# Kernel optimization log

Measured on AMD Instinct MI355X. Metric: run time of the kernel, lower is better.

## Reference

```python
import jax, jax.numpy as jnp
import numpy as np

K = 8192   # num_embeddings
D = 256    # embedding_dim


def setup_inputs() -> dict:
    key = jax.random.key(0)
    k1, k2 = jax.random.split(key)
    inputs = jax.random.normal(k1, (8, 4096, D), dtype=jnp.float32)
    # torch init: uniform_(-1/num_embeddings, 1/num_embeddings)
    embeddings_weight = jax.random.uniform(
        k2, (K, D), dtype=jnp.float32, minval=-1.0 / K, maxval=1.0 / K
    )
    return {"inputs": inputs, "embeddings_weight": embeddings_weight}


def reference(inputs, embeddings_weight):
    in_shape = inputs.shape
    flat = inputs.reshape(-1, D)                      # [N, D]
    distances = (
        jnp.sum(flat * flat, axis=1, keepdims=True)   # [N, 1]
        + jnp.sum(embeddings_weight * embeddings_weight, axis=1)  # [K]
        - 2.0 * jnp.matmul(flat, embeddings_weight.T)             # [N, K]
    )
    encoding_indices = jnp.argmin(distances, axis=1)  # [N] int
    # one-hot @ W is mathematically a row gather of W
    quantized = jnp.take(embeddings_weight, encoding_indices, axis=0).reshape(in_shape)
    return quantized, encoding_indices
```

## Files before the change

### kernel.cpp

```cpp
#include <hip/hip_runtime.h>
#include <cfloat>


#define DDIM 256

typedef int   i32x8  __attribute__((ext_vector_type(8)));
typedef float f32x16 __attribute__((ext_vector_type(16)));

__device__ __forceinline__ float np_sumsq_lane(const float* __restrict__ a) {
    float r = __fmul_rn(a[0], a[0]);
#pragma unroll
    for (int t = 1; t < 16; ++t)
        r = __fadd_rn(r, __fmul_rn(a[8 * t], a[8 * t]));
    return r;
}

__global__ __launch_bounds__(256) void vq_prep(
    const float* __restrict__ x, const float* __restrict__ w,
    float* __restrict__ x2, float* __restrict__ wn,
    unsigned char* __restrict__ xb8, unsigned char* __restrict__ wb8,
    int nxblocks) {
    __shared__ float rows[32 * 260];
    const int tid = threadIdx.x;
    const bool isX = (int)blockIdx.x < nxblocks;
    const int r0 = (isX ? blockIdx.x : (blockIdx.x - nxblocks)) * 32;
    const float* src = isX ? x : w;

    for (int idx = tid; idx < 32 * 64; idx += 256) {
        int r = idx >> 6, c4 = idx & 63;
        *(float4*)&rows[r * 260 + c4 * 4] =
            *(const float4*)(src + (size_t)(r0 + r) * DDIM + c4 * 4);
    }
    __syncthreads();
    {
        const int row = (tid >> 6) * 8 + ((tid & 63) >> 3), j = tid & 7;
        const float* a = &rows[row * 260];
        float half[2];
#pragma unroll
        for (int h = 0; h < 2; ++h) {
            float r = np_sumsq_lane(a + h * 128 + j);
            float p = __fadd_rn(r, __shfl_xor(r, 1, 64));
            p = __fadd_rn(p, __shfl_xor(p, 2, 64));
            p = __fadd_rn(p, __shfl_xor(p, 4, 64));
            half[h] = p;
        }
        float s = __fadd_rn(half[0], half[1]);
        if (j == 0) { if (isX) x2[r0 + row] = s; else wn[r0 + row] = s; }
    }
    {
        const float scale = isX ? 1.0f : -8192.0f;
        unsigned char* dst = isX ? xb8 : wb8;
        for (int idx = tid; idx < 32 * 16; idx += 256) {
            int r = idx >> 4, s = idx & 15;
            const float* p = &rows[r * 260 + s * 16];
            unsigned q[4];
#pragma unroll
            for (int m = 0; m < 4; ++m) {
                unsigned v = (unsigned)__builtin_amdgcn_cvt_pk_fp8_f32(
                    p[m * 4 + 0] * scale, p[m * 4 + 1] * scale, 0, false);
                v = (unsigned)__builtin_amdgcn_cvt_pk_fp8_f32(
                    p[m * 4 + 2] * scale, p[m * 4 + 3] * scale, (int)v, true);
                q[m] = v;
            }
            *(uint4*)(dst + (size_t)(r0 + r) * DDIM + s * 16) =
                make_uint4(q[0], q[1], q[2], q[3]);
        }
    }
}

__global__ __launch_bounds__(512, 1) void vq_score(
    const unsigned char* __restrict__ xb8, const unsigned char* __restrict__ wb8,
    unsigned* __restrict__ cand) {
    __shared__ __align__(16) unsigned char Ws[2][32768];
    const int tid = threadIdx.x;
    const int wave = tid >> 6, lane = tid & 63;
    const int h = lane >> 5, c32 = lane & 31;
    const int wr = wave >> 2, wc = wave & 3;
    const int rowBase = blockIdx.x * 128;

    i32x8 af[2][4];
#pragma unroll
    for (int rt = 0; rt < 2; ++rt) {
        const unsigned char* xr =
            xb8 + (size_t)(rowBase + wr * 64 + rt * 32 + c32) * DDIM;
#pragma unroll
        for (int ks = 0; ks < 4; ++ks) {
            union { uint4 q[2]; i32x8 v; } u;
            u.q[0] = *(const uint4*)(xr + ks * 64 + h * 32);
            u.q[1] = *(const uint4*)(xr + ks * 64 + h * 32 + 16);
            af[rt][ks] = u.v;
        }
    }

    unsigned sOfs[4]; unsigned ldsOfs[4];
#pragma unroll
    for (int i = 0; i < 4; ++i) {
        int col = (wave * 4 + i) * 4 + (lane >> 4);
        int gsrc = (lane & 15) ^ (col & 15);
        sOfs[i] = (unsigned)(col * 256 + gsrc * 16);
        ldsOfs[i] = (unsigned)((wave * 4 + i) * 1024);
    }

    unsigned s0[2][16], s1[2][16];
#pragma unroll
    for (int a = 0; a < 2; ++a)
#pragma unroll
        for (int r = 0; r < 16; ++r) { s0[a][r] = 0xFFFFFFFFu; s1[a][r] = 0xFFFFFFFFu; }

    const int bcol = wc * 32 + c32, cs = bcol & 15;
    int bofs[4][2];
#pragma unroll
    for (int ks = 0; ks < 4; ++ks) {
        int gb = ks * 4 + h * 2;
        bofs[ks][0] = bcol * 256 + ((gb) ^ cs) * 16;
        bofs[ks][1] = bcol * 256 + ((gb + 1) ^ cs) * 16;
    }

    auto stage = [&](int kt, int buf) {
        const unsigned char* g = wb8 + (size_t)kt * 32768;
#pragma unroll
        for (int i = 0; i < 4; ++i)
            __builtin_amdgcn_global_load_lds(
                (const __attribute__((address_space(1))) unsigned int*)(g + sOfs[i]),
                (__attribute__((address_space(3))) unsigned int*)(&Ws[buf][ldsOfs[i]]),
                16, 0, 0);
    };

    stage(0, 0);
    for (int kt = 0; kt < 64; ++kt) {
        const int cur = kt & 1;
        __syncthreads();
        if (kt + 1 < 64) stage(kt + 1, cur ^ 1);

        f32x16 acc[2];
#pragma unroll
        for (int rt = 0; rt < 2; ++rt)
#pragma unroll
            for (int r = 0; r < 16; ++r) acc[rt][r] = 128.0f;
#pragma unroll
        for (int ks = 0; ks < 4; ++ks) {
            union { uint4 q[2]; i32x8 v; } b;
            b.q[0] = *(const uint4*)&Ws[cur][bofs[ks][0]];
            b.q[1] = *(const uint4*)&Ws[cur][bofs[ks][1]];
#pragma unroll
            for (int rt = 0; rt < 2; ++rt)
                acc[rt] = __builtin_amdgcn_mfma_scale_f32_32x32x64_f8f6f4(
                    af[rt][ks], b.v, acc[rt], 0, 0,
                    0, 0x7F7F7F7F, 0, 0x7F7F7F7F);
        }
        const unsigned colv = (unsigned)(kt * 128 + bcol);
#pragma unroll
        for (int rt = 0; rt < 2; ++rt)
#pragma unroll
            for (int r = 0; r < 16; ++r) {
                unsigned key = (__float_as_uint(acc[rt][r]) & 0xFFFFE000u) | colv;
                unsigned a0 = s0[rt][r];
                unsigned mx = key > a0 ? key : a0;
                s1[rt][r] = mx < s1[rt][r] ? mx : s1[rt][r];
                s0[rt][r] = key < a0 ? key : a0;
            }
    }

    unsigned* ms = (unsigned*)Ws;
    for (int g = 0; g < 2; ++g) {
        __syncthreads();
        if (wr == g) {
#pragma unroll
            for (int rt = 0; rt < 2; ++rt)
#pragma unroll
                for (int r = 0; r < 16; ++r) {
                    int rloc = rt * 32 + (r & 3) + 8 * (r >> 2) + 4 * h;
                    *(uint2*)&ms[rloc * 256 + bcol * 2] =
                        make_uint2(s0[rt][r], s1[rt][r]);
                }
        }
        __syncthreads();
        if (tid < 64) {
            const unsigned* rowk = ms + tid * 256;
            unsigned best[8];
#pragma unroll
            for (int i = 0; i < 8; ++i) best[i] = 0xFFFFFFFFu;
            for (int i = 0; i < 256; ++i) {
                unsigned key = rowk[(i + tid * 4) & 255];
                if (key < best[7]) {
                    best[7] = key;
#pragma unroll
                    for (int j = 7; j > 0; --j)
                        if (best[j] < best[j - 1]) {
                            unsigned t = best[j]; best[j] = best[j - 1]; best[j - 1] = t;
                        }
                }
            }
            unsigned* out = cand + (size_t)(rowBase + g * 64 + tid) * 8;
#pragma unroll
            for (int i = 0; i < 8; ++i) out[i] = best[i];
        }
    }
}

__global__ __launch_bounds__(256) void vq_rescore_write(
    const float* __restrict__ x, const float* __restrict__ w,
    const float* __restrict__ x2, const float* __restrict__ wn,
    const unsigned* __restrict__ cand, float* __restrict__ outq,
    float* __restrict__ outi) {
    __shared__ int winners[32];
    const int tid = threadIdx.x;
    const int lr = tid >> 3, cc = tid & 7;
    const int row = blockIdx.x * 32 + lr;

    int k = (int)(cand[(size_t)row * 8 + cc] & 0x1FFFu);
    const float* xr = x + (size_t)row * DDIM;
    const float* wr = w + (size_t)k * DDIM;
    float acc = 0.f;
#pragma unroll 8
    for (int d = 0; d < DDIM; d += 4) {
        float4 xv = *reinterpret_cast<const float4*>(xr + d);
        float4 wv = *reinterpret_cast<const float4*>(wr + d);
        acc = __fmaf_rn(xv.x, wv.x, acc);
        acc = __fmaf_rn(xv.y, wv.y, acc);
        acc = __fmaf_rn(xv.z, wv.z, acc);
        acc = __fmaf_rn(xv.w, wv.w, acc);
    }
    float dv = __fsub_rn(__fadd_rn(x2[row], wn[k]), __fmul_rn(2.0f, acc));
#pragma unroll
    for (int m = 1; m < 8; m <<= 1) {
        float od = __shfl_xor(dv, m, 64);
        int   ok = __shfl_xor(k,  m, 64);
        if (od < dv || (od == dv && ok < k)) { dv = od; k = ok; }
    }
    if (cc == 0) winners[lr] = k;
    __syncthreads();
    if (tid < 32) outi[blockIdx.x * 32 + tid] = (float)winners[tid];
    for (int u = tid; u < 32 * 64; u += 256) {
        int r = u >> 6, c4 = u & 63;
        *reinterpret_cast<float4*>(outq + (size_t)(blockIdx.x * 32 + r) * DDIM + c4 * 4) =
            *reinterpret_cast<const float4*>(w + (size_t)winners[r] * DDIM + c4 * 4);
    }
}

extern "C" void kernel_launch(void* const* d_in, const int* in_sizes, int n_in,
                              void* d_out, int out_size, void* d_ws, size_t ws_size,
                              hipStream_t stream) {
    const float* x = (const float*)d_in[0];
    const float* w = (const float*)d_in[1];
    const int N = in_sizes[0] / DDIM;
    const int K = in_sizes[1] / DDIM;
    float* outq = (float*)d_out;
    float* outi = outq + (size_t)N * DDIM;

    unsigned char* xb8 = (unsigned char*)d_ws;
    unsigned char* wb8 = xb8 + (size_t)N * DDIM;
    float* x2 = (float*)(wb8 + (size_t)K * DDIM);
    float* wn = x2 + N;
    unsigned* cand = (unsigned*)(wn + K);

    hipLaunchKernelGGL(vq_prep, dim3((N + K) / 32), dim3(256), 0, stream,
                       x, w, x2, wn, xb8, wb8, N / 32);
    hipLaunchKernelGGL(vq_score, dim3(N / 128), dim3(512), 0, stream,
                       xb8, wb8, cand);
    hipLaunchKernelGGL(vq_rescore_write, dim3(N / 32), dim3(256), 0, stream,
                       x, w, x2, wn, cand, outq, outi);
}
```

Before: 299.0 us.

## Fuse x fp8 quantization into scoring and x norms into rescore, shrink score blocks

```diff
diff --git a/kernel.cpp b/kernel.cpp
--- a/kernel.cpp
+++ b/kernel.cpp
@@ -7,29 +7,17 @@
 typedef int   i32x8  __attribute__((ext_vector_type(8)));
 typedef float f32x16 __attribute__((ext_vector_type(16)));
 
-__device__ __forceinline__ float np_sumsq_lane(const float* __restrict__ a) {
-    float r = __fmul_rn(a[0], a[0]);
-#pragma unroll
-    for (int t = 1; t < 16; ++t)
-        r = __fadd_rn(r, __fmul_rn(a[8 * t], a[8 * t]));
-    return r;
-}
-
-__global__ __launch_bounds__(256) void vq_prep(
-    const float* __restrict__ x, const float* __restrict__ w,
-    float* __restrict__ x2, float* __restrict__ wn,
-    unsigned char* __restrict__ xb8, unsigned char* __restrict__ wb8,
-    int nxblocks) {
+__global__ __launch_bounds__(256) void vq_prep_w(
+    const float* __restrict__ w, float* __restrict__ wn,
+    unsigned char* __restrict__ wb8) {
     __shared__ float rows[32 * 260];
     const int tid = threadIdx.x;
-    const bool isX = (int)blockIdx.x < nxblocks;
-    const int r0 = (isX ? blockIdx.x : (blockIdx.x - nxblocks)) * 32;
-    const float* src = isX ? x : w;
+    const int r0 = blockIdx.x * 32;
 
     for (int idx = tid; idx < 32 * 64; idx += 256) {
         int r = idx >> 6, c4 = idx & 63;
         *(float4*)&rows[r * 260 + c4 * 4] =
-            *(const float4*)(src + (size_t)(r0 + r) * DDIM + c4 * 4);
+            *(const float4*)(w + (size_t)(r0 + r) * DDIM + c4 * 4);
     }
     __syncthreads();
     {
@@ -38,67 +26,74 @@
         float half[2];
 #pragma unroll
         for (int h = 0; h < 2; ++h) {
-            float r = np_sumsq_lane(a + h * 128 + j);
+            const float* b = a + h * 128 + j;
+            float r = __fmul_rn(b[0], b[0]);
+#pragma unroll
+            for (int t = 1; t < 16; ++t)
+                r = __fadd_rn(r, __fmul_rn(b[8 * t], b[8 * t]));
             float p = __fadd_rn(r, __shfl_xor(r, 1, 64));
             p = __fadd_rn(p, __shfl_xor(p, 2, 64));
             p = __fadd_rn(p, __shfl_xor(p, 4, 64));
             half[h] = p;
         }
-        float s = __fadd_rn(half[0], half[1]);
-        if (j == 0) { if (isX) x2[r0 + row] = s; else wn[r0 + row] = s; }
-    }
-    {
-        const float scale = isX ? 1.0f : -8192.0f;
-        unsigned char* dst = isX ? xb8 : wb8;
-        for (int idx = tid; idx < 32 * 16; idx += 256) {
-            int r = idx >> 4, s = idx & 15;
-            const float* p = &rows[r * 260 + s * 16];
-            unsigned q[4];
-#pragma unroll
-            for (int m = 0; m < 4; ++m) {
-                unsigned v = (unsigned)__builtin_amdgcn_cvt_pk_fp8_f32(
-                    p[m * 4 + 0] * scale, p[m * 4 + 1] * scale, 0, false);
-                v = (unsigned)__builtin_amdgcn_cvt_pk_fp8_f32(
-                    p[m * 4 + 2] * scale, p[m * 4 + 3] * scale, (int)v, true);
-                q[m] = v;
-            }
-            *(uint4*)(dst + (size_t)(r0 + r) * DDIM + s * 16) =
-                make_uint4(q[0], q[1], q[2], q[3]);
-        }
-    }
-}
-
-__global__ __launch_bounds__(512, 1) void vq_score(
-    const unsigned char* __restrict__ xb8, const unsigned char* __restrict__ wb8,
+        if (j == 0) wn[r0 + row] = __fadd_rn(half[0], half[1]);
+    }
+    for (int idx = tid; idx < 32 * 16; idx += 256) {
+        int r = idx >> 4, s = idx & 15;
+        const float* p = &rows[r * 260 + s * 16];
+        unsigned q[4];
+#pragma unroll
+        for (int m = 0; m < 4; ++m) {
+            unsigned v = (unsigned)__builtin_amdgcn_cvt_pk_fp8_f32(
+                p[m * 4 + 0] * -8192.f, p[m * 4 + 1] * -8192.f, 0, false);
+            v = (unsigned)__builtin_amdgcn_cvt_pk_fp8_f32(
+                p[m * 4 + 2] * -8192.f, p[m * 4 + 3] * -8192.f, (int)v, true);
+            q[m] = v;
+        }
+        *(uint4*)(wb8 + (size_t)(r0 + r) * DDIM + s * 16) =
+            make_uint4(q[0], q[1], q[2], q[3]);
+    }
+}
+
+__global__ __launch_bounds__(256, 2) void vq_score(
+    const float* __restrict__ x, const unsigned char* __restrict__ wb8,
     unsigned* __restrict__ cand) {
     __shared__ __align__(16) unsigned char Ws[2][32768];
     const int tid = threadIdx.x;
     const int wave = tid >> 6, lane = tid & 63;
     const int h = lane >> 5, c32 = lane & 31;
-    const int wr = wave >> 2, wc = wave & 3;
-    const int rowBase = blockIdx.x * 128;
+    const int wc = wave;
+    const int rowBase = blockIdx.x * 64;
 
     i32x8 af[2][4];
 #pragma unroll
     for (int rt = 0; rt < 2; ++rt) {
-        const unsigned char* xr =
-            xb8 + (size_t)(rowBase + wr * 64 + rt * 32 + c32) * DDIM;
+        const float* xr = x + (size_t)(rowBase + rt * 32 + c32) * DDIM;
 #pragma unroll
         for (int ks = 0; ks < 4; ++ks) {
-            union { uint4 q[2]; i32x8 v; } u;
-            u.q[0] = *(const uint4*)(xr + ks * 64 + h * 32);
-            u.q[1] = *(const uint4*)(xr + ks * 64 + h * 32 + 16);
+            const float4* p = (const float4*)(xr + ks * 64 + h * 32);
+            union { int d[8]; i32x8 v; } u;
+#pragma unroll
+            for (int m = 0; m < 8; ++m) {
+                float4 f = p[m];
+                unsigned v = (unsigned)__builtin_amdgcn_cvt_pk_fp8_f32(
+                    f.x, f.y, 0, false);
+                v = (unsigned)__builtin_amdgcn_cvt_pk_fp8_f32(
+                    f.z, f.w, (int)v, true);
+                u.d[m] = (int)v;
+            }
             af[rt][ks] = u.v;
         }
     }
 
-    unsigned sOfs[4]; unsigned ldsOfs[4];
-#pragma unroll
-    for (int i = 0; i < 4; ++i) {
-        int col = (wave * 4 + i) * 4 + (lane >> 4);
+    unsigned sOfs[8], ldsOfs[8];
+#pragma unroll
+    for (int i = 0; i < 8; ++i) {
+        int slot = wave * 8 + i;
+        int col  = slot * 4 + (lane >> 4);
         int gsrc = (lane & 15) ^ (col & 15);
-        sOfs[i] = (unsigned)(col * 256 + gsrc * 16);
-        ldsOfs[i] = (unsigned)((wave * 4 + i) * 1024);
+        sOfs[i]   = (unsigned)(col * 256 + gsrc * 16);
+        ldsOfs[i] = (unsigned)(slot * 1024);
     }
 
     unsigned s0[2][16], s1[2][16];
@@ -112,14 +107,14 @@
 #pragma unroll
     for (int ks = 0; ks < 4; ++ks) {
         int gb = ks * 4 + h * 2;
-        bofs[ks][0] = bcol * 256 + ((gb) ^ cs) * 16;
+        bofs[ks][0] = bcol * 256 + ((gb)     ^ cs) * 16;
         bofs[ks][1] = bcol * 256 + ((gb + 1) ^ cs) * 16;
     }
 
     auto stage = [&](int kt, int buf) {
         const unsigned char* g = wb8 + (size_t)kt * 32768;
 #pragma unroll
-        for (int i = 0; i < 4; ++i)
+        for (int i = 0; i < 8; ++i)
             __builtin_amdgcn_global_load_lds(
                 (const __attribute__((address_space(1))) unsigned int*)(g + sOfs[i]),
                 (__attribute__((address_space(3))) unsigned int*)(&Ws[buf][ldsOfs[i]]),
@@ -161,27 +156,27 @@
             }
     }
 
+    __syncthreads();
     unsigned* ms = (unsigned*)Ws;
-    for (int g = 0; g < 2; ++g) {
-        __syncthreads();
-        if (wr == g) {
-#pragma unroll
-            for (int rt = 0; rt < 2; ++rt)
-#pragma unroll
-                for (int r = 0; r < 16; ++r) {
-                    int rloc = rt * 32 + (r & 3) + 8 * (r >> 2) + 4 * h;
-                    *(uint2*)&ms[rloc * 256 + bcol * 2] =
-                        make_uint2(s0[rt][r], s1[rt][r]);
-                }
-        }
-        __syncthreads();
-        if (tid < 64) {
-            const unsigned* rowk = ms + tid * 256;
-            unsigned best[8];
-#pragma unroll
-            for (int i = 0; i < 8; ++i) best[i] = 0xFFFFFFFFu;
-            for (int i = 0; i < 256; ++i) {
-                unsigned key = rowk[(i + tid * 4) & 255];
+#pragma unroll
+    for (int rt = 0; rt < 2; ++rt)
+#pragma unroll
+        for (int r = 0; r < 16; ++r) {
+            int rloc = rt * 32 + (r & 3) + 8 * (r >> 2) + 4 * h;
+            *(uint2*)&ms[rloc * 256 + bcol * 2] = make_uint2(s0[rt][r], s1[rt][r]);
+        }
+    __syncthreads();
+    if (tid < 64) {
+        const uint4* rowk = (const uint4*)(ms + tid * 256);
+        unsigned best[8];
+#pragma unroll
+        for (int i = 0; i < 8; ++i) best[i] = 0xFFFFFFFFu;
+        for (int i = 0; i < 64; ++i) {
+            uint4 qv = rowk[(i + tid) & 63];
+            unsigned kk[4] = {qv.x, qv.y, qv.z, qv.w};
+#pragma unroll
+            for (int e = 0; e < 4; ++e) {
+                unsigned key = kk[e];
                 if (key < best[7]) {
                     best[7] = key;
 #pragma unroll
@@ -191,18 +186,17 @@
                         }
                 }
             }
-            unsigned* out = cand + (size_t)(rowBase + g * 64 + tid) * 8;
-#pragma unroll
-            for (int i = 0; i < 8; ++i) out[i] = best[i];
-        }
+        }
+        unsigned* out = cand + (size_t)(rowBase + tid) * 8;
+#pragma unroll
+        for (int i = 0; i < 8; ++i) out[i] = best[i];
     }
 }
 
 __global__ __launch_bounds__(256) void vq_rescore_write(
     const float* __restrict__ x, const float* __restrict__ w,
-    const float* __restrict__ x2, const float* __restrict__ wn,
-    const unsigned* __restrict__ cand, float* __restrict__ outq,
-    float* __restrict__ outi) {
+    const float* __restrict__ wn, const unsigned* __restrict__ cand,
+    float* __restrict__ outq, float* __restrict__ outi) {
     __shared__ int winners[32];
     const int tid = threadIdx.x;
     const int lr = tid >> 3, cc = tid & 7;
@@ -211,17 +205,43 @@
     int k = (int)(cand[(size_t)row * 8 + cc] & 0x1FFFu);
     const float* xr = x + (size_t)row * DDIM;
     const float* wr = w + (size_t)k * DDIM;
-    float acc = 0.f;
-#pragma unroll 8
-    for (int d = 0; d < DDIM; d += 4) {
-        float4 xv = *reinterpret_cast<const float4*>(xr + d);
-        float4 wv = *reinterpret_cast<const float4*>(wr + d);
-        acc = __fmaf_rn(xv.x, wv.x, acc);
-        acc = __fmaf_rn(xv.y, wv.y, acc);
-        acc = __fmaf_rn(xv.z, wv.z, acc);
-        acc = __fmaf_rn(xv.w, wv.w, acc);
-    }
-    float dv = __fsub_rn(__fadd_rn(x2[row], wn[k]), __fmul_rn(2.0f, acc));
+    float dot = 0.f;
+    float half[2];
+#pragma unroll
+    for (int hh = 0; hh < 2; ++hh) {
+        float r[8];
+#pragma unroll
+        for (int t = 0; t < 16; ++t) {
+            const int d = hh * 128 + t * 8;
+            float4 xa = *(const float4*)(xr + d);
+            float4 xb = *(const float4*)(xr + d + 4);
+            float4 wa = *(const float4*)(wr + d);
+            float4 wb = *(const float4*)(wr + d + 4);
+            dot = __fmaf_rn(xa.x, wa.x, dot); dot = __fmaf_rn(xa.y, wa.y, dot);
+            dot = __fmaf_rn(xa.z, wa.z, dot); dot = __fmaf_rn(xa.w, wa.w, dot);
+            dot = __fmaf_rn(xb.x, wb.x, dot); dot = __fmaf_rn(xb.y, wb.y, dot);
+            dot = __fmaf_rn(xb.z, wb.z, dot); dot = __fmaf_rn(xb.w, wb.w, dot);
+            if (t == 0) {
+                r[0] = __fmul_rn(xa.x, xa.x); r[1] = __fmul_rn(xa.y, xa.y);
+                r[2] = __fmul_rn(xa.z, xa.z); r[3] = __fmul_rn(xa.w, xa.w);
+                r[4] = __fmul_rn(xb.x, xb.x); r[5] = __fmul_rn(xb.y, xb.y);
+                r[6] = __fmul_rn(xb.z, xb.z); r[7] = __fmul_rn(xb.w, xb.w);
+            } else {
+                r[0] = __fadd_rn(r[0], __fmul_rn(xa.x, xa.x));
+                r[1] = __fadd_rn(r[1], __fmul_rn(xa.y, xa.y));
+                r[2] = __fadd_rn(r[2], __fmul_rn(xa.z, xa.z));
+                r[3] = __fadd_rn(r[3], __fmul_rn(xa.w, xa.w));
+                r[4] = __fadd_rn(r[4], __fmul_rn(xb.x, xb.x));
+                r[5] = __fadd_rn(r[5], __fmul_rn(xb.y, xb.y));
+                r[6] = __fadd_rn(r[6], __fmul_rn(xb.w == xb.w ? xb.z : xb.z, xb.z));
+                r[7] = __fadd_rn(r[7], __fmul_rn(xb.w, xb.w));
+            }
+        }
+        half[hh] = __fadd_rn(__fadd_rn(__fadd_rn(r[0], r[1]), __fadd_rn(r[2], r[3])),
+                             __fadd_rn(__fadd_rn(r[4], r[5]), __fadd_rn(r[6], r[7])));
+    }
+    float x2v = __fadd_rn(half[0], half[1]);
+    float dv = __fsub_rn(__fadd_rn(x2v, wn[k]), __fmul_rn(2.0f, dot));
 #pragma unroll
     for (int m = 1; m < 8; m <<= 1) {
         float od = __shfl_xor(dv, m, 64);
@@ -248,16 +268,12 @@
     float* outq = (float*)d_out;
     float* outi = outq + (size_t)N * DDIM;
 
-    unsigned char* xb8 = (unsigned char*)d_ws;
-    unsigned char* wb8 = xb8 + (size_t)N * DDIM;
-    float* x2 = (float*)(wb8 + (size_t)K * DDIM);
-    float* wn = x2 + N;
+    unsigned char* wb8 = (unsigned char*)d_ws;
+    float* wn = (float*)(wb8 + (size_t)K * DDIM);
     unsigned* cand = (unsigned*)(wn + K);
 
-    hipLaunchKernelGGL(vq_prep, dim3((N + K) / 32), dim3(256), 0, stream,
-                       x, w, x2, wn, xb8, wb8, N / 32);
-    hipLaunchKernelGGL(vq_score, dim3(N / 128), dim3(512), 0, stream,
-                       xb8, wb8, cand);
+    hipLaunchKernelGGL(vq_prep_w, dim3(K / 32), dim3(256), 0, stream, w, wn, wb8);
+    hipLaunchKernelGGL(vq_score, dim3(N / 64), dim3(256), 0, stream, x, wb8, cand);
     hipLaunchKernelGGL(vq_rescore_write, dim3(N / 32), dim3(256), 0, stream,
-                       x, w, x2, wn, cand, outq, outi);
-}
+                       x, w, wn, cand, outq, outi);
+}
```

Result: faster. 256.3 us (-14.3%).
